# Kernel optimization log

Hardware: AMD Instinct MI355X
Metric: run time of the kernel (lower is better)

The kernel has to match this reference:

```python
import jax, jax.numpy as jnp
import numpy as np

N, C, H, W_ = 256, 64, 32, 32
IN_F = H * W_   # 1024
OUT_F = 1024

def setup_inputs() -> dict:
    key = jax.random.key(0)
    k1, k2, k3 = jax.random.split(key, 3)
    x = jax.random.normal(k1, (N, C, H, W_), dtype=jnp.float32)
    # per-channel Linear weights: (C, out_features, in_features), bias (C, out_features)
    scale = 1.0 / np.sqrt(IN_F)
    W = jax.random.uniform(k2, (C, OUT_F, IN_F), dtype=jnp.float32, minval=-scale, maxval=scale)
    b = jax.random.uniform(k3, (C, OUT_F), dtype=jnp.float32, minval=-scale, maxval=scale)
    return {"x": x, "W": W, "b": b}

def reference(x, W, b):
    n, c = x.shape[0], x.shape[1]
    z = x.reshape(n, c, -1)                      # (N, C, X)
    # sort each channel's vector in descending order (sort=True)
    z = -jnp.sort(-z, axis=-1)
    # grouped per-channel GEMM: y[n,c,o] = sum_x z[n,c,x] * W[c,o,x] + b[c,o]
    y = jnp.einsum('ncx,cox->nco', z, W) + b[None, :, :]
    return jax.nn.sigmoid(y)
```

## Files before the change

### kernel.cpp

```cpp
#include <hip/hip_runtime.h>

typedef _Float16 half8   __attribute__((ext_vector_type(8)));
typedef __fp16   half2_t __attribute__((ext_vector_type(2)));
typedef float    floatx4 __attribute__((ext_vector_type(4)));

__device__ inline void async_copy16(const void* g, void* l) {
  __builtin_amdgcn_global_load_lds(
      (const __attribute__((address_space(1))) unsigned int*)g,
      (__attribute__((address_space(3))) unsigned int*)l, 16, 0, 0);
}

__global__ __launch_bounds__(256) void sort_kernel(const float* __restrict__ x,
                                                   unsigned short* __restrict__ zs) {
  const int wave = threadIdx.x >> 6;
  const int lane = threadIdx.x & 63;
  const int vec  = (blockIdx.x << 2) + wave;

  const float* src = x + ((size_t)vec << 10) + (lane << 4);
  float v[16];
#pragma unroll
  for (int r4 = 0; r4 < 4; ++r4) {
    float4 f = *reinterpret_cast<const float4*>(src + (r4 << 2));
    v[r4 * 4 + 0] = f.x; v[r4 * 4 + 1] = f.y;
    v[r4 * 4 + 2] = f.z; v[r4 * 4 + 3] = f.w;
  }

  auto CEs = [&](int a, int b, bool desc) {
    float lo = fminf(v[a], v[b]);
    float hi = fmaxf(v[a], v[b]);
    v[a] = desc ? hi : lo;
    v[b] = desc ? lo : hi;
  };

#pragma unroll
  for (int r = 0; r < 16; r += 2) CEs(r, r + 1, (r & 2) == 0);
#pragma unroll
  for (int r = 0; r < 16; ++r) if ((r & 2) == 0) CEs(r, r | 2, (r & 4) == 0);
#pragma unroll
  for (int r = 0; r < 16; r += 2) CEs(r, r + 1, (r & 4) == 0);
#pragma unroll
  for (int r = 0; r < 16; ++r) if ((r & 4) == 0) CEs(r, r | 4, (r & 8) == 0);
#pragma unroll
  for (int r = 0; r < 16; ++r) if ((r & 2) == 0) CEs(r, r | 2, (r & 8) == 0);
#pragma unroll
  for (int r = 0; r < 16; r += 2) CEs(r, r + 1, (r & 8) == 0);

#pragma unroll
  for (int k = 16; k <= 1024; k <<= 1) {
    const bool d = (lane & (k >> 4)) == 0;
#pragma unroll
    for (int j = k >> 1; j >= 16; j >>= 1) {
      const int dl = j >> 4;
      const bool keepmax = (((lane & dl) == 0) == d);
#pragma unroll
      for (int r = 0; r < 16; ++r) {
        float p = __shfl_xor(v[r], dl, 64);
        v[r] = keepmax ? fmaxf(v[r], p) : fminf(v[r], p);
      }
    }
#pragma unroll
    for (int j = 8; j >= 1; j >>= 1)
#pragma unroll
      for (int r = 0; r < 16; ++r)
        if ((r & j) == 0) CEs(r, r | j, d);
  }

  const int n = vec >> 6, c = vec & 63;
  union { half2_t h2[8]; uint4 u[2]; } pk;
#pragma unroll
  for (int r = 0; r < 8; ++r)
    pk.h2[r] = __builtin_amdgcn_cvt_pkrtz(v[2 * r], v[2 * r + 1]);
  uint4* dst = reinterpret_cast<uint4*>(zs + ((size_t)(c * 256 + n) << 10) + (lane << 4));
  dst[0] = pk.u[0];
  dst[1] = pk.u[1];
}

__global__ __launch_bounds__(256) void gemm_kernel(const unsigned short* __restrict__ zs,
                                                   const float* __restrict__ W,
                                                   const float* __restrict__ bias,
                                                   float* __restrict__ out) {
  __shared__ unsigned short As[256 * 64];
  __shared__ float          Bs[64 * 64];

  const int c    = blockIdx.y;
  const int nt   = blockIdx.x;
  const int tid  = threadIdx.x;
  const int w    = tid >> 6, lane = tid & 63;
  const int lr   = lane & 15;
  const int q    = lane >> 4;

  const unsigned short* zc = zs + (((size_t)c * 256) << 10);
  const float*          wc = W + ((size_t)c << 20) + (((size_t)nt * 64) << 10);

  const int a_lr8 = lane >> 3, a_ch = lane & 7;
  const int a_cs  = a_ch ^ a_lr8;
  const int b_lr4 = lane >> 4, b_ch = lane & 15;
  const int b_cs  = b_ch ^ ((4 * (w & 1) + b_lr4) & 7);

  floatx4 acc[4][4] = {};
  union U { uint4 u; half8 h; float4 f; };

  for (int kb = 0; kb < 1024; kb += 64) {
#pragma unroll
    for (int p = 0; p < 8; ++p) {
      const int r0 = (p * 4 + w) * 8;
      const unsigned short* g =
          zc + (((size_t)(r0 + a_lr8)) << 10) + kb + (a_cs << 3);
      async_copy16(g, &As[r0 << 6]);
    }
#pragma unroll
    for (int p = 0; p < 4; ++p) {
      const int o0 = (p * 4 + w) * 4;
      const float* g = wc + (((size_t)(o0 + b_lr4)) << 10) + kb + (b_cs << 2);
      async_copy16(g, &Bs[o0 << 6]);
    }
    __syncthreads();

#pragma unroll
    for (int ks = 0; ks < 2; ++ks) {
      half8 af[4];
#pragma unroll
      for (int mi = 0; mi < 4; ++mi) {
        const int r  = w * 64 + mi * 16 + lr;
        const int ch = (ks * 4 + q) ^ (r & 7);
        af[mi] = *reinterpret_cast<const half8*>(&As[(r << 6) + (ch << 3)]);
      }
#pragma unroll
      for (int ni = 0; ni < 4; ++ni) {
        const int o  = ni * 16 + lr;
        const int c0 = (ks * 8 + q * 2) ^ (o & 7);
        const int c1 = (ks * 8 + q * 2 + 1) ^ (o & 7);
        const float4 f0 = *reinterpret_cast<const float4*>(&Bs[(o << 6) + (c0 << 2)]);
        const float4 f1 = *reinterpret_cast<const float4*>(&Bs[(o << 6) + (c1 << 2)]);
        union { half2_t h2[4]; half8 h8; } pk;
        pk.h2[0] = __builtin_amdgcn_cvt_pkrtz(f0.x, f0.y);
        pk.h2[1] = __builtin_amdgcn_cvt_pkrtz(f0.z, f0.w);
        pk.h2[2] = __builtin_amdgcn_cvt_pkrtz(f1.x, f1.y);
        pk.h2[3] = __builtin_amdgcn_cvt_pkrtz(f1.z, f1.w);
#pragma unroll
        for (int mi = 0; mi < 4; ++mi)
          acc[mi][ni] =
              __builtin_amdgcn_mfma_f32_16x16x32_f16(af[mi], pk.h8, acc[mi][ni], 0, 0, 0);
      }
    }
    __syncthreads();
  }

#pragma unroll
  for (int ni = 0; ni < 4; ++ni) {
    const int col = nt * 64 + ni * 16 + lr;
    const float bv = bias[(c << 10) + col];
#pragma unroll
    for (int mi = 0; mi < 4; ++mi) {
      const int row0 = w * 64 + mi * 16 + q * 4;
#pragma unroll
      for (int rr = 0; rr < 4; ++rr) {
        const float y = acc[mi][ni][rr] + bv;
        const float s = __builtin_amdgcn_rcpf(1.0f + __expf(-y));
        out[(((size_t)(row0 + rr) << 6) + c) * 1024 + col] = s;
      }
    }
  }
}

extern "C" void kernel_launch(void* const* d_in, const int* in_sizes, int n_in,
                              void* d_out, int out_size, void* d_ws, size_t ws_size,
                              hipStream_t stream) {
  const float* x    = (const float*)d_in[0];
  const float* W    = (const float*)d_in[1];
  const float* bias = (const float*)d_in[2];
  float*       out  = (float*)d_out;
  unsigned short* zs = (unsigned short*)d_ws;

  sort_kernel<<<4096, 256, 0, stream>>>(x, zs);
  gemm_kernel<<<dim3(16, 64), 256, 0, stream>>>(zs, W, bias, out);
}
```

Baseline: 482.8 us.

## Restructure GEMM with larger tiles, register-prefetched fp16 B double buffer, direct A loads

The GEMM tile per block grows from 256x64 to 256x128, using a 2x2 wave layout with 8x4 MFMA accumulators per wave. W is prefetched into registers, converted to fp16 once, and written into a double-buffered swizzled LDS buffer, so the fp32-to-fp16 conversion is no longer repeated per fragment. The A operand is read straight from global memory instead of being staged in LDS. The grid becomes 1D with a channel-interleaved block order, and launch bounds target two blocks per CU. The risks are higher register pressure and uncoalesced, latency-exposed direct global loads for A.

```diff
diff --git a/kernel.cpp b/kernel.cpp
--- a/kernel.cpp
+++ b/kernel.cpp
@@ -3,12 +3,6 @@
 typedef _Float16 half8   __attribute__((ext_vector_type(8)));
 typedef __fp16   half2_t __attribute__((ext_vector_type(2)));
 typedef float    floatx4 __attribute__((ext_vector_type(4)));
-
-__device__ inline void async_copy16(const void* g, void* l) {
-  __builtin_amdgcn_global_load_lds(
-      (const __attribute__((address_space(1))) unsigned int*)g,
-      (__attribute__((address_space(3))) unsigned int*)l, 16, 0, 0);
-}
 
 __global__ __launch_bounds__(256) void sort_kernel(const float* __restrict__ x,
                                                    unsigned short* __restrict__ zs) {
@@ -75,89 +69,100 @@
   dst[1] = pk.u[1];
 }
 
-__global__ __launch_bounds__(256) void gemm_kernel(const unsigned short* __restrict__ zs,
-                                                   const float* __restrict__ W,
-                                                   const float* __restrict__ bias,
-                                                   float* __restrict__ out) {
-  __shared__ unsigned short As[256 * 64];
-  __shared__ float          Bs[64 * 64];
+__global__ __launch_bounds__(256, 2) void gemm_kernel(const unsigned short* __restrict__ zs,
+                                                      const float* __restrict__ W,
+                                                      const float* __restrict__ bias,
+                                                      float* __restrict__ out) {
+  __shared__ __align__(16) _Float16 Bs[2][128 * 64];
 
-  const int c    = blockIdx.y;
-  const int nt   = blockIdx.x;
+  const int bid = blockIdx.x;
+  const int c   = ((bid & 7) << 3) | ((bid >> 3) & 7);
+  const int nt  = bid >> 6;
   const int tid  = threadIdx.x;
-  const int w    = tid >> 6, lane = tid & 63;
-  const int lr   = lane & 15;
-  const int q    = lane >> 4;
+  const int w = tid >> 6, lane = tid & 63;
+  const int lr = lane & 15, q = lane >> 4;
+  const int wm = w >> 1, wn = w & 1;
 
-  const unsigned short* zc = zs + (((size_t)c * 256) << 10);
-  const float*          wc = W + ((size_t)c << 20) + (((size_t)nt * 64) << 10);
+  const unsigned short* zc = zs + ((size_t)c << 18);
+  const float*          wc = W + ((size_t)c << 20) + ((size_t)nt << 17);
 
-  const int a_lr8 = lane >> 3, a_ch = lane & 7;
-  const int a_cs  = a_ch ^ a_lr8;
-  const int b_lr4 = lane >> 4, b_ch = lane & 15;
-  const int b_cs  = b_ch ^ ((4 * (w & 1) + b_lr4) & 7);
+  const int so = (w << 3) + (lane >> 3);
+  const int sc = lane & 7;
+  const unsigned short* arow = zc + (((size_t)((wm << 7) + lr)) << 10) + (q << 3);
 
-  floatx4 acc[4][4] = {};
-  union U { uint4 u; half8 h; float4 f; };
+  floatx4 acc[8][4] = {};
+  float4  breg[8];
 
-  for (int kb = 0; kb < 1024; kb += 64) {
-#pragma unroll
-    for (int p = 0; p < 8; ++p) {
-      const int r0 = (p * 4 + w) * 8;
-      const unsigned short* g =
-          zc + (((size_t)(r0 + a_lr8)) << 10) + kb + (a_cs << 3);
-      async_copy16(g, &As[r0 << 6]);
-    }
+  auto loadB = [&](int kb) {
 #pragma unroll
     for (int p = 0; p < 4; ++p) {
-      const int o0 = (p * 4 + w) * 4;
-      const float* g = wc + (((size_t)(o0 + b_lr4)) << 10) + kb + (b_cs << 2);
-      async_copy16(g, &Bs[o0 << 6]);
+      const int o = (p << 5) + so;
+      const float* g = wc + ((size_t)o << 10) + kb + (sc << 3);
+      breg[2 * p]     = *reinterpret_cast<const float4*>(g);
+      breg[2 * p + 1] = *reinterpret_cast<const float4*>(g + 4);
     }
+  };
+  auto writeB = [&](int buf) {
+#pragma unroll
+    for (int p = 0; p < 4; ++p) {
+      const int o = (p << 5) + so;
+      union { half2_t h2[4]; half8 h8; } pk;
+      const float4 f0 = breg[2 * p], f1 = breg[2 * p + 1];
+      pk.h2[0] = __builtin_amdgcn_cvt_pkrtz(f0.x, f0.y);
+      pk.h2[1] = __builtin_amdgcn_cvt_pkrtz(f0.z, f0.w);
+      pk.h2[2] = __builtin_amdgcn_cvt_pkrtz(f1.x, f1.y);
+      pk.h2[3] = __builtin_amdgcn_cvt_pkrtz(f1.z, f1.w);
+      *reinterpret_cast<half8*>(&Bs[buf][(o << 6) + ((sc ^ (o & 7)) << 3)]) = pk.h8;
+    }
+  };
+  auto compute = [&](int buf, int kb, int ks) {
+    half8 af[8];
+#pragma unroll
+    for (int mi = 0; mi < 8; ++mi)
+      af[mi] = *reinterpret_cast<const half8*>(arow + (mi << 14) + kb + (ks << 5));
+#pragma unroll
+    for (int ni = 0; ni < 4; ++ni) {
+      const int o  = (wn << 6) + (ni << 4) + lr;
+      const int ch = ((ks << 2) + q) ^ (o & 7);
+      const half8 bf = *reinterpret_cast<const half8*>(&Bs[buf][(o << 6) + (ch << 3)]);
+#pragma unroll
+      for (int mi = 0; mi < 8; ++mi)
+        acc[mi][ni] =
+            __builtin_amdgcn_mfma_f32_16x16x32_f16(af[mi], bf, acc[mi][ni], 0, 0, 0);
+    }
+  };
+
+  loadB(0);
+  writeB(0);
+  __syncthreads();
+
+#pragma unroll 1
+  for (int t = 0; t < 8; ++t) {
+    const int kb = t << 7;
+    loadB(kb + 64);
+    compute(0, kb, 0);
+    writeB(1);
+    compute(0, kb, 1);
     __syncthreads();
-
-#pragma unroll
-    for (int ks = 0; ks < 2; ++ks) {
-      half8 af[4];
-#pragma unroll
-      for (int mi = 0; mi < 4; ++mi) {
-        const int r  = w * 64 + mi * 16 + lr;
-        const int ch = (ks * 4 + q) ^ (r & 7);
-        af[mi] = *reinterpret_cast<const half8*>(&As[(r << 6) + (ch << 3)]);
-      }
-#pragma unroll
-      for (int ni = 0; ni < 4; ++ni) {
-        const int o  = ni * 16 + lr;
-        const int c0 = (ks * 8 + q * 2) ^ (o & 7);
-        const int c1 = (ks * 8 + q * 2 + 1) ^ (o & 7);
-        const float4 f0 = *reinterpret_cast<const float4*>(&Bs[(o << 6) + (c0 << 2)]);
-        const float4 f1 = *reinterpret_cast<const float4*>(&Bs[(o << 6) + (c1 << 2)]);
-        union { half2_t h2[4]; half8 h8; } pk;
-        pk.h2[0] = __builtin_amdgcn_cvt_pkrtz(f0.x, f0.y);
-        pk.h2[1] = __builtin_amdgcn_cvt_pkrtz(f0.z, f0.w);
-        pk.h2[2] = __builtin_amdgcn_cvt_pkrtz(f1.x, f1.y);
-        pk.h2[3] = __builtin_amdgcn_cvt_pkrtz(f1.z, f1.w);
-#pragma unroll
-        for (int mi = 0; mi < 4; ++mi)
-          acc[mi][ni] =
-              __builtin_amdgcn_mfma_f32_16x16x32_f16(af[mi], pk.h8, acc[mi][ni], 0, 0, 0);
-      }
-    }
+    if (t < 7) loadB(kb + 128);
+    compute(1, kb + 64, 0);
+    if (t < 7) writeB(0);
+    compute(1, kb + 64, 1);
     __syncthreads();
   }
 
 #pragma unroll
   for (int ni = 0; ni < 4; ++ni) {
-    const int col = nt * 64 + ni * 16 + lr;
+    const int col = (nt << 7) + (wn << 6) + (ni << 4) + lr;
     const float bv = bias[(c << 10) + col];
 #pragma unroll
-    for (int mi = 0; mi < 4; ++mi) {
-      const int row0 = w * 64 + mi * 16 + q * 4;
+    for (int mi = 0; mi < 8; ++mi) {
+      const int row0 = (wm << 7) + (mi << 4) + (q << 2);
 #pragma unroll
       for (int rr = 0; rr < 4; ++rr) {
         const float y = acc[mi][ni][rr] + bv;
         const float s = __builtin_amdgcn_rcpf(1.0f + __expf(-y));
-        out[(((size_t)(row0 + rr) << 6) + c) * 1024 + col] = s;
+        out[((((size_t)(row0 + rr) << 6) | c) << 10) + col] = s;
       }
     }
   }
@@ -173,5 +178,5 @@
   unsigned short* zs = (unsigned short*)d_ws;
 
   sort_kernel<<<4096, 256, 0, stream>>>(x, zs);
-  gemm_kernel<<<dim3(16, 64), 256, 0, stream>>>(zs, W, bias, out);
+  gemm_kernel<<<512, 256, 0, stream>>>(zs, W, bias, out);
 }
```

Result: slower. 530.5 us (+9.9%).
